# Kernel tuning notes

Measured on AMD Instinct MI355X. Metric: run time of the kernel, lower is better.

The kernel has to match this reference:

```python
import jax, jax.numpy as jnp
import numpy as np

EMBED_DIM = 1024
NUM_HEADS = 16
HEAD_DIM = EMBED_DIM // NUM_HEADS
SCALE = HEAD_DIM ** -0.5


def setup_inputs() -> dict:
    key = jax.random.key(0)
    ks = jax.random.split(key, 11)
    B, T, C = 4, 2048, EMBED_DIM
    s = 1.0 / np.sqrt(C)
    return {
        "query": jax.random.normal(ks[0], (B, T, C), jnp.float32),
        "key": jax.random.normal(ks[1], (B, T, C), jnp.float32),
        "value": jax.random.normal(ks[2], (B, T, C), jnp.float32),
        "Wq": jax.random.normal(ks[3], (C, C), jnp.float32) * s,
        "bq": jnp.zeros((C,), jnp.float32),
        "Wk": jax.random.normal(ks[4], (C, C), jnp.float32) * s,
        "bk": jnp.zeros((C,), jnp.float32),
        "Wv": jax.random.normal(ks[5], (C, C), jnp.float32) * s,
        "bv": jnp.zeros((C,), jnp.float32),
        "Wo": jax.random.normal(ks[6], (C, C), jnp.float32) * s,
        "bo": jnp.zeros((C,), jnp.float32),
    }


def reference(query, key, value, Wq, bq, Wk, bk, Wv, bv, Wo, bo):
    B, Tq, C = query.shape
    Tk = key.shape[1]
    H, D = NUM_HEADS, HEAD_DIM
    # Linear projections (torch Linear: x @ W.T + b), split heads -> (B, H, T, D)
    q = (query @ Wq.T + bq).reshape(B, Tq, H, D).transpose(0, 2, 1, 3)
    k = (key @ Wk.T + bk).reshape(B, Tk, H, D).transpose(0, 2, 1, 3)
    v = (value @ Wv.T + bv).reshape(B, Tk, H, D).transpose(0, 2, 1, 3)
    scores = jnp.einsum("bhqd,bhkd->bhqk", q, k) * SCALE
    attn = jax.nn.softmax(scores, axis=-1)
    out = jnp.einsum("bhqk,bhkd->bhqd", attn, v)
    out = out.transpose(0, 2, 1, 3).reshape(B, Tq, C)
    return out @ Wo.T + bo
```

## Files before the change

kernel.cpp:

```cpp
#include <hip/hip_runtime.h>
#include <stdint.h>
#include <math.h>

#define C_DIM 1024
#define H_NUM 16
#define D_DIM 64
#define B_NUM 4
#define T_SEQ 2048
#define M_ROWS (B_NUM * T_SEQ)

#define SCALE_LOG2E (0.125f * 1.44269504088896340736f)

typedef __attribute__((ext_vector_type(8))) __bf16 bf16x8;
typedef __attribute__((ext_vector_type(2))) __bf16 bf16x2;
typedef __attribute__((ext_vector_type(4))) float f32x4;

__device__ __forceinline__ unsigned short f2bf(float f) {
  union { float f; uint32_t u; } v; v.f = f;
  uint32_t r = v.u + 0x7FFFu + ((v.u >> 16) & 1u);
  return (unsigned short)(r >> 16);
}

__device__ __forceinline__ uint32_t pk2bf(float a, float b) {
#if __has_builtin(__builtin_amdgcn_cvt_pk_bf16_f32)
  union { bf16x2 v; uint32_t u; } u;
  u.v = __builtin_amdgcn_cvt_pk_bf16_f32(a, b);
  return u.u;
#else
  union { float f; uint32_t u; } x, y; x.f = a; y.f = b;
  return __builtin_amdgcn_perm(y.u + 0x8000u, x.u + 0x8000u, 0x07060302u);
#endif
}

__device__ __forceinline__ float frcp(float x) {
#if __has_builtin(__builtin_amdgcn_rcpf)
  return __builtin_amdgcn_rcpf(x);
#else
  return 1.f / x;
#endif
}

__device__ __forceinline__ f32x4 mfma16(bf16x8 a, bf16x8 b, f32x4 c) {
  return __builtin_amdgcn_mfma_f32_16x16x32_bf16(a, b, c, 0, 0, 0);
}

__device__ __forceinline__ void cp16(const void* g, void* l) {
  __builtin_amdgcn_global_load_lds(
      (const __attribute__((address_space(1))) unsigned int*)g,
      (__attribute__((address_space(3))) unsigned int*)l, 16, 0, 0);
}

__global__ __launch_bounds__(256) void cast_all(
    const float* __restrict__ a0, const float* __restrict__ a1,
    const float* __restrict__ a2, const float* __restrict__ w0,
    const float* __restrict__ w1, const float* __restrict__ w2,
    const float* __restrict__ w3, unsigned short* __restrict__ oa0,
    unsigned short* __restrict__ oa1, unsigned short* __restrict__ oa2,
    unsigned short* __restrict__ ow0, unsigned short* __restrict__ ow1,
    unsigned short* __restrict__ ow2, unsigned short* __restrict__ ow3,
    int big4, int small4) {
  int i = blockIdx.x * 256 + threadIdx.x;
  int y = blockIdx.y;
  const float* s;
  unsigned short* d;
  int n4;
  switch (y) {
    case 0: s = a0; d = oa0; n4 = big4; break;
    case 1: s = a1; d = oa1; n4 = big4; break;
    case 2: s = a2; d = oa2; n4 = big4; break;
    case 3: s = w0; d = ow0; n4 = small4; break;
    case 4: s = w1; d = ow1; n4 = small4; break;
    case 5: s = w2; d = ow2; n4 = small4; break;
    default: s = w3; d = ow3; n4 = small4; break;
  }
  if (i >= n4) return;
  float4 v = ((const float4*)s)[i];
  ushort4 o;
  o.x = f2bf(v.x); o.y = f2bf(v.y); o.z = f2bf(v.z); o.w = f2bf(v.w);
  ((ushort4*)d)[i] = o;
}

__device__ __forceinline__ void gemm_tile_128(
    const unsigned short* __restrict__ A, const unsigned short* __restrict__ Bw,
    int row0, int col0, unsigned short* As, unsigned short* Bs, f32x4 acc[4][4]) {
  const int lane = threadIdx.x & 63;
  const int wave = threadIdx.x >> 6;
  const int wm = wave >> 1, wn = wave & 1;
#pragma unroll
  for (int mt = 0; mt < 4; ++mt)
#pragma unroll
    for (int nt = 0; nt < 4; ++nt) acc[mt][nt] = (f32x4){0.f, 0.f, 0.f, 0.f};

  for (int k0 = 0; k0 < C_DIM; k0 += 64) {
    __syncthreads();
#pragma unroll
    for (int rr = 0; rr < 4; ++rr) {
      int c = (rr * 4 + wave) * 64 + lane;
      int row = c >> 3;
      int g = (c & 7) ^ (row & 7);
      cp16(A + (size_t)(row0 + row) * C_DIM + k0 + g * 8, As + (rr * 4 + wave) * 512);
      cp16(Bw + (size_t)(col0 + row) * C_DIM + k0 + g * 8, Bs + (rr * 4 + wave) * 512);
    }
    __syncthreads();
#pragma unroll
    for (int ks = 0; ks < 2; ++ks) {
      bf16x8 af[4], bfr[4];
#pragma unroll
      for (int mt = 0; mt < 4; ++mt) {
        int row = wm * 64 + mt * 16 + (lane & 15);
        int gs = (ks * 4 + (lane >> 4)) ^ (row & 7);
        af[mt] = *(const bf16x8*)(As + row * 64 + gs * 8);
      }
#pragma unroll
      for (int nt = 0; nt < 4; ++nt) {
        int row = wn * 64 + nt * 16 + (lane & 15);
        int gs = (ks * 4 + (lane >> 4)) ^ (row & 7);
        bfr[nt] = *(const bf16x8*)(Bs + row * 64 + gs * 8);
      }
#pragma unroll
      for (int mt = 0; mt < 4; ++mt)
#pragma unroll
        for (int nt = 0; nt < 4; ++nt)
          acc[mt][nt] = mfma16(af[mt], bfr[nt], acc[mt][nt]);
    }
  }
}

__global__ __launch_bounds__(256) void gemm_qkv(
    const unsigned short* __restrict__ qb, const unsigned short* __restrict__ kb,
    const unsigned short* __restrict__ vb, const unsigned short* __restrict__ wq,
    const unsigned short* __restrict__ wk, const unsigned short* __restrict__ wv,
    const float* __restrict__ bq, const float* __restrict__ bk,
    const float* __restrict__ bv, unsigned short* __restrict__ Qp,
    unsigned short* __restrict__ Kp, unsigned short* __restrict__ Vp) {
  __shared__ alignas(16) unsigned short As[128 * 64];
  __shared__ alignas(16) unsigned short Bs[128 * 64];
  const int z = blockIdx.z;
  const unsigned short* A = (z == 0) ? qb : (z == 1) ? kb : vb;
  const unsigned short* W = (z == 0) ? wq : (z == 1) ? wk : wv;
  const float* bias = (z == 0) ? bq : (z == 1) ? bk : bv;
  const int row0 = blockIdx.y * 128, col0 = blockIdx.x * 128;
  f32x4 acc[4][4];
  gemm_tile_128(A, W, row0, col0, As, Bs, acc);

  const int lane = threadIdx.x & 63;
  const int wave = threadIdx.x >> 6;
  const int wm = wave >> 1, wn = wave & 1;
  const int quad = lane >> 4;
#pragma unroll
  for (int mt = 0; mt < 4; ++mt)
#pragma unroll
    for (int nt = 0; nt < 4; ++nt) {
      int n = col0 + wn * 64 + nt * 16 + (lane & 15);
      float bval = bias[n];
      int h = n >> 6, d = n & 63;
      if (z == 2) {
        int m0 = row0 + wm * 64 + mt * 16 + quad * 4;
        int b = m0 >> 11, t0 = m0 & 2047;
        float f0 = acc[mt][nt][0] + bval, f1 = acc[mt][nt][1] + bval;
        float f2 = acc[mt][nt][2] + bval, f3 = acc[mt][nt][3] + bval;
        uint2 pk = {pk2bf(f0, f1), pk2bf(f2, f3)};
        size_t off = (((size_t)(b * H_NUM + h) * (T_SEQ / 8) + (t0 >> 3)) * D_DIM + d) * 8
                     + (t0 & 7);
        *(uint2*)(Vp + off) = pk;
      } else {
#pragma unroll
        for (int r = 0; r < 4; ++r) {
          int m = row0 + wm * 64 + mt * 16 + quad * 4 + r;
          int b = m >> 11, t = m & 2047;
          float f = acc[mt][nt][r] + bval;
          if (z == 0) f *= SCALE_LOG2E;
          unsigned short val = f2bf(f);
          if (z == 0)
            Qp[((size_t)(b * H_NUM + h) * T_SEQ + t) * D_DIM + d] = val;
          else
            Kp[((size_t)(b * H_NUM + h) * T_SEQ + t) * D_DIM + d] = val;
        }
      }
    }
}

__device__ __forceinline__ int fsw(int r) { return (r + ((r >> 3) << 2)) & 7; }

__global__ __launch_bounds__(256, 3) void attn_kernel(
    const unsigned short* __restrict__ Qp, const unsigned short* __restrict__ Kp,
    const unsigned short* __restrict__ Vp, unsigned short* __restrict__ Op) {
  __shared__ alignas(16) unsigned short Ks[2][64 * 64];
  __shared__ alignas(16) unsigned short Vt[2][64 * 64];
  const int bh = blockIdx.x;
  const int q0 = blockIdx.y * 128;
  const int lane = threadIdx.x & 63;
  const int wave = threadIdx.x >> 6;
  const int quad = lane >> 4;
  const int q15 = lane & 15;

  bf16x8 qf[2][2];
#pragma unroll
  for (int g = 0; g < 2; ++g) {
    const unsigned short* qrow =
        Qp + ((size_t)bh * T_SEQ + q0 + wave * 32 + g * 16 + q15) * D_DIM;
    qf[g][0] = *(const bf16x8*)(qrow + quad * 8);
    qf[g][1] = *(const bf16x8*)(qrow + 32 + quad * 8);
  }

  bf16x8 onesf;
#pragma unroll
  for (int i = 0; i < 8; ++i) onesf[i] = (__bf16)1.0f;

  f32x4 oacc[2][4];
  f32x4 lacc[2];
#pragma unroll
  for (int g = 0; g < 2; ++g) {
    lacc[g] = (f32x4){0.f, 0.f, 0.f, 0.f};
#pragma unroll
    for (int dt = 0; dt < 4; ++dt) oacc[g][dt] = (f32x4){0.f, 0.f, 0.f, 0.f};
  }

  const unsigned short* Kbase = Kp + (size_t)bh * T_SEQ * D_DIM;
  const unsigned short* Vbase = Vp + (size_t)bh * T_SEQ * D_DIM;

#define STAGE(kt, buf)                                                        \
  {                                                                           \
    _Pragma("unroll") for (int i = 0; i < 2; ++i) {                           \
      int chunk = wave * 2 + i;                                     \
      int c = chunk * 64 + lane;                                              \
      int row = c >> 3;                                                       \
      int g = (c & 7) ^ fsw(row);                                             \
      cp16(Kbase + ((size_t)((kt) * 64 + row)) * D_DIM + g * 8,               \
           &Ks[buf][chunk * 512]);                                            \
      cp16(Vbase + (size_t)((kt) * 8 + chunk) * 512 + lane * 8,               \
           &Vt[buf][chunk * 512]);                                            \
    }                                                                         \
  }

  STAGE(0, 0);

  for (int kt = 0; kt < T_SEQ / 64; ++kt) {
    const int buf = kt & 1;
    __syncthreads();
    if (kt + 1 < T_SEQ / 64) STAGE(kt + 1, buf ^ 1);

    bf16x8 kfr[4][2];
#pragma unroll
    for (int mt = 0; mt < 4; ++mt) {
      int rowp = 32 * (mt >> 1) + (q15 >> 2) * 8 + (mt & 1) * 4 + (q15 & 3);
#pragma unroll
      for (int ks = 0; ks < 2; ++ks) {
        int gs = (ks * 4 + quad) ^ fsw(rowp);
        kfr[mt][ks] = *(const bf16x8*)(&Ks[buf][rowp * 64 + gs * 8]);
      }
    }
    bf16x8 Pb[2][2];
#pragma unroll
    for (int g = 0; g < 2; ++g) {
      f32x4 s[4];
#pragma unroll
      for (int mt = 0; mt < 4; ++mt) s[mt] = (f32x4){0.f, 0.f, 0.f, 0.f};
#pragma unroll
      for (int ks = 0; ks < 2; ++ks)
#pragma unroll
        for (int mt = 0; mt < 4; ++mt)
          s[mt] = mfma16(kfr[mt][ks], qf[g][ks], s[mt]);
#pragma unroll
      for (int a = 0; a < 2; ++a) {
        float p0 = __builtin_amdgcn_exp2f(s[2 * a][0]);
        float p1 = __builtin_amdgcn_exp2f(s[2 * a][1]);
        float p2 = __builtin_amdgcn_exp2f(s[2 * a][2]);
        float p3 = __builtin_amdgcn_exp2f(s[2 * a][3]);
        float p4 = __builtin_amdgcn_exp2f(s[2 * a + 1][0]);
        float p5 = __builtin_amdgcn_exp2f(s[2 * a + 1][1]);
        float p6 = __builtin_amdgcn_exp2f(s[2 * a + 1][2]);
        float p7 = __builtin_amdgcn_exp2f(s[2 * a + 1][3]);
        union { bf16x8 v; uint32_t u[4]; } pk;
        pk.u[0] = pk2bf(p0, p1);
        pk.u[1] = pk2bf(p2, p3);
        pk.u[2] = pk2bf(p4, p5);
        pk.u[3] = pk2bf(p6, p7);
        Pb[g][a] = pk.v;
      }
    }

#pragma unroll
    for (int a = 0; a < 2; ++a) {
      lacc[0] = mfma16(onesf, Pb[0][a], lacc[0]);
      lacc[1] = mfma16(onesf, Pb[1][a], lacc[1]);
#pragma unroll
      for (int dt = 0; dt < 4; ++dt) {
        bf16x8 vf =
            *(const bf16x8*)(&Vt[buf][((a * 4 + quad) * 64 + dt * 16 + q15) * 8]);
        oacc[0][dt] = mfma16(vf, Pb[0][a], oacc[0][dt]);
        oacc[1][dt] = mfma16(vf, Pb[1][a], oacc[1][dt]);
      }
    }
  }
#undef STAGE

  const int b = bh >> 4, h = bh & 15;
#pragma unroll
  for (int g = 0; g < 2; ++g) {
    float inv = frcp(lacc[g][0]);
    int t = q0 + wave * 32 + g * 16 + q15;
#pragma unroll
    for (int dt = 0; dt < 4; ++dt) {
      uint2 o = {pk2bf(oacc[g][dt][0] * inv, oacc[g][dt][1] * inv),
                 pk2bf(oacc[g][dt][2] * inv, oacc[g][dt][3] * inv)};
      int col = h * D_DIM + dt * 16 + quad * 4;
      *(uint2*)(Op + ((size_t)b * T_SEQ + t) * C_DIM + col) = o;
    }
  }
}

__global__ __launch_bounds__(256) void gemm_out_kernel(
    const unsigned short* __restrict__ Op, const unsigned short* __restrict__ wo,
    const float* __restrict__ bo, float* __restrict__ out) {
  __shared__ alignas(16) unsigned short As[128 * 64];
  __shared__ alignas(16) unsigned short Bs[128 * 64];
  const int row0 = blockIdx.y * 128, col0 = blockIdx.x * 128;
  f32x4 acc[4][4];
  gemm_tile_128(Op, wo, row0, col0, As, Bs, acc);

  const int lane = threadIdx.x & 63;
  const int wave = threadIdx.x >> 6;
  const int wm = wave >> 1, wn = wave & 1;
#pragma unroll
  for (int mt = 0; mt < 4; ++mt)
#pragma unroll
    for (int nt = 0; nt < 4; ++nt) {
      int n = col0 + wn * 64 + nt * 16 + (lane & 15);
      float bval = bo[n];
#pragma unroll
      for (int r = 0; r < 4; ++r) {
        int m = row0 + wm * 64 + mt * 16 + (lane >> 4) * 4 + r;
        out[(size_t)m * C_DIM + n] = acc[mt][nt][r] + bval;
      }
    }
}

extern "C" void kernel_launch(void* const* d_in, const int* in_sizes, int n_in,
                              void* d_out, int out_size, void* d_ws, size_t ws_size,
                              hipStream_t stream) {
  const float* q_in = (const float*)d_in[0];
  const float* k_in = (const float*)d_in[1];
  const float* v_in = (const float*)d_in[2];
  const float* Wq = (const float*)d_in[3];
  const float* bq = (const float*)d_in[4];
  const float* Wk = (const float*)d_in[5];
  const float* bk = (const float*)d_in[6];
  const float* Wv = (const float*)d_in[7];
  const float* bv = (const float*)d_in[8];
  const float* Wo = (const float*)d_in[9];
  const float* bo = (const float*)d_in[10];
  float* out = (float*)d_out;

  const size_t MC = (size_t)M_ROWS * C_DIM;
  const size_t CC = (size_t)C_DIM * C_DIM;
  unsigned short* qb = (unsigned short*)d_ws;
  unsigned short* kb = qb + MC;
  unsigned short* vb = kb + MC;
  unsigned short* wqb = vb + MC;
  unsigned short* wkb = wqb + CC;
  unsigned short* wvb = wkb + CC;
  unsigned short* wob = wvb + CC;
  unsigned short* Qp = wob + CC;
  unsigned short* Kp = Qp + MC;
  unsigned short* Vp = Kp + MC;
  unsigned short* Op = Vp + MC;

  const int big4 = (int)(MC / 4), small4 = (int)(CC / 4);
  cast_all<<<dim3((big4 + 255) / 256, 7), dim3(256), 0, stream>>>(
      q_in, k_in, v_in, Wq, Wk, Wv, Wo, qb, kb, vb, wqb, wkb, wvb, wob,
      big4, small4);

  gemm_qkv<<<dim3(C_DIM / 128, M_ROWS / 128, 3), dim3(256), 0, stream>>>(
      qb, kb, vb, wqb, wkb, wvb, bq, bk, bv, Qp, Kp, Vp);

  attn_kernel<<<dim3(B_NUM * H_NUM, T_SEQ / 128), dim3(256), 0, stream>>>(
      Qp, Kp, Vp, Op);

  gemm_out_kernel<<<dim3(C_DIM / 128, M_ROWS / 128), dim3(256), 0, stream>>>(
      Op, wob, bo, out);
}
```

Before: 334.3 us.

## Double-buffer GEMM LDS tiles, remap block order, transpose Q/K epilogue

The shared GEMM tile loop now uses two LDS buffers, issuing the async copy for the next K-slice before computing on the current one, with a single barrier per iteration so loads overlap MFMA work. Both GEMM kernels remap the linear block index so consecutive blocks share the same weight column tile and spread across row tiles, aiming for better L2 reuse. For Q and K projections the operands are swapped so each lane holds four consecutive head-dim values, allowing packed 8-byte stores and a vectorized bias load instead of scattered 2-byte stores. LDS use doubles to 64KB per block, which may reduce occupancy.

```diff
diff --git a/kernel.cpp b/kernel.cpp
--- a/kernel.cpp
+++ b/kernel.cpp
@@ -91,17 +91,26 @@
 #pragma unroll
     for (int nt = 0; nt < 4; ++nt) acc[mt][nt] = (f32x4){0.f, 0.f, 0.f, 0.f};
 
-  for (int k0 = 0; k0 < C_DIM; k0 += 64) {
+#define GQSTAGE(kk, bb)                                                        \
+  {                                                                            \
+    _Pragma("unroll") for (int rr = 0; rr < 4; ++rr) {                         \
+      int c = (rr * 4 + wave) * 64 + lane;                                     \
+      int row = c >> 3;                                                        \
+      int g = (c & 7) ^ (row & 7);                                             \
+      cp16(A + (size_t)(row0 + row) * C_DIM + (kk) + g * 8,                    \
+           As + (bb) * 8192 + (rr * 4 + wave) * 512);                          \
+      cp16(Bw + (size_t)(col0 + row) * C_DIM + (kk) + g * 8,                   \
+           Bs + (bb) * 8192 + (rr * 4 + wave) * 512);                          \
+    }                                                                          \
+  }
+
+  GQSTAGE(0, 0);
+  for (int it = 0; it < C_DIM / 64; ++it) {
+    const int buf = it & 1;
     __syncthreads();
-#pragma unroll
-    for (int rr = 0; rr < 4; ++rr) {
-      int c = (rr * 4 + wave) * 64 + lane;
-      int row = c >> 3;
-      int g = (c & 7) ^ (row & 7);
-      cp16(A + (size_t)(row0 + row) * C_DIM + k0 + g * 8, As + (rr * 4 + wave) * 512);
-      cp16(Bw + (size_t)(col0 + row) * C_DIM + k0 + g * 8, Bs + (rr * 4 + wave) * 512);
-    }
-    __syncthreads();
+    if (it + 1 < C_DIM / 64) GQSTAGE((it + 1) * 64, buf ^ 1);
+    const unsigned short* Ab = As + buf * 8192;
+    const unsigned short* Bb = Bs + buf * 8192;
 #pragma unroll
     for (int ks = 0; ks < 2; ++ks) {
       bf16x8 af[4], bfr[4];
@@ -109,13 +118,13 @@
       for (int mt = 0; mt < 4; ++mt) {
         int row = wm * 64 + mt * 16 + (lane & 15);
         int gs = (ks * 4 + (lane >> 4)) ^ (row & 7);
-        af[mt] = *(const bf16x8*)(As + row * 64 + gs * 8);
+        af[mt] = *(const bf16x8*)(Ab + row * 64 + gs * 8);
       }
 #pragma unroll
       for (int nt = 0; nt < 4; ++nt) {
         int row = wn * 64 + nt * 16 + (lane & 15);
         int gs = (ks * 4 + (lane >> 4)) ^ (row & 7);
-        bfr[nt] = *(const bf16x8*)(Bs + row * 64 + gs * 8);
+        bfr[nt] = *(const bf16x8*)(Bb + row * 64 + gs * 8);
       }
 #pragma unroll
       for (int mt = 0; mt < 4; ++mt)
@@ -124,6 +133,7 @@
           acc[mt][nt] = mfma16(af[mt], bfr[nt], acc[mt][nt]);
     }
   }
+#undef GQSTAGE
 }
 
 __global__ __launch_bounds__(256) void gemm_qkv(
@@ -133,51 +143,64 @@
     const float* __restrict__ bq, const float* __restrict__ bk,
     const float* __restrict__ bv, unsigned short* __restrict__ Qp,
     unsigned short* __restrict__ Kp, unsigned short* __restrict__ Vp) {
-  __shared__ alignas(16) unsigned short As[128 * 64];
-  __shared__ alignas(16) unsigned short Bs[128 * 64];
-  const int z = blockIdx.z;
+  __shared__ alignas(16) unsigned short As[2][128 * 64];
+  __shared__ alignas(16) unsigned short Bs[2][128 * 64];
+  const int lin = blockIdx.x + 8 * blockIdx.y + 512 * blockIdx.z;
+  const int rowb = ((lin & 7) << 3) | ((lin >> 3) & 7);
+  const int colb = (lin >> 6) & 7;
+  const int z = lin >> 9;
   const unsigned short* A = (z == 0) ? qb : (z == 1) ? kb : vb;
   const unsigned short* W = (z == 0) ? wq : (z == 1) ? wk : wv;
   const float* bias = (z == 0) ? bq : (z == 1) ? bk : bv;
-  const int row0 = blockIdx.y * 128, col0 = blockIdx.x * 128;
-  f32x4 acc[4][4];
-  gemm_tile_128(A, W, row0, col0, As, Bs, acc);
+  const int m0 = rowb * 128, n0 = colb * 128;
 
   const int lane = threadIdx.x & 63;
   const int wave = threadIdx.x >> 6;
   const int wm = wave >> 1, wn = wave & 1;
   const int quad = lane >> 4;
-#pragma unroll
-  for (int mt = 0; mt < 4; ++mt)
-#pragma unroll
-    for (int nt = 0; nt < 4; ++nt) {
-      int n = col0 + wn * 64 + nt * 16 + (lane & 15);
-      float bval = bias[n];
-      int h = n >> 6, d = n & 63;
-      if (z == 2) {
-        int m0 = row0 + wm * 64 + mt * 16 + quad * 4;
-        int b = m0 >> 11, t0 = m0 & 2047;
+  const int q15 = lane & 15;
+  f32x4 acc[4][4];
+
+  if (z == 2) {
+    gemm_tile_128(A, W, m0, n0, &As[0][0], &Bs[0][0], acc);
+#pragma unroll
+    for (int mt = 0; mt < 4; ++mt)
+#pragma unroll
+      for (int nt = 0; nt < 4; ++nt) {
+        int n = n0 + wn * 64 + nt * 16 + q15;
+        float bval = bias[n];
+        int h = n >> 6, d = n & 63;
+        int m0t = m0 + wm * 64 + mt * 16 + quad * 4;
+        int b = m0t >> 11, t0 = m0t & 2047;
         float f0 = acc[mt][nt][0] + bval, f1 = acc[mt][nt][1] + bval;
         float f2 = acc[mt][nt][2] + bval, f3 = acc[mt][nt][3] + bval;
         uint2 pk = {pk2bf(f0, f1), pk2bf(f2, f3)};
         size_t off = (((size_t)(b * H_NUM + h) * (T_SEQ / 8) + (t0 >> 3)) * D_DIM + d) * 8
                      + (t0 & 7);
         *(uint2*)(Vp + off) = pk;
-      } else {
-#pragma unroll
-        for (int r = 0; r < 4; ++r) {
-          int m = row0 + wm * 64 + mt * 16 + quad * 4 + r;
-          int b = m >> 11, t = m & 2047;
-          float f = acc[mt][nt][r] + bval;
-          if (z == 0) f *= SCALE_LOG2E;
-          unsigned short val = f2bf(f);
-          if (z == 0)
-            Qp[((size_t)(b * H_NUM + h) * T_SEQ + t) * D_DIM + d] = val;
-          else
-            Kp[((size_t)(b * H_NUM + h) * T_SEQ + t) * D_DIM + d] = val;
-        }
-      }
-    }
+      }
+  } else {
+    gemm_tile_128(W, A, n0, m0, &As[0][0], &Bs[0][0], acc);
+    unsigned short* dst = (z == 0) ? Qp : Kp;
+    const float sc = (z == 0) ? SCALE_LOG2E : 1.0f;
+#pragma unroll
+    for (int mt = 0; mt < 4; ++mt) {
+      int nb = n0 + wm * 64 + mt * 16 + quad * 4;
+      float4 b4 = *(const float4*)(bias + nb);
+      int h = nb >> 6, d0 = nb & 63;
+#pragma unroll
+      for (int nt = 0; nt < 4; ++nt) {
+        int m = m0 + wn * 64 + nt * 16 + q15;
+        int b = m >> 11, t = m & 2047;
+        float f0 = (acc[mt][nt][0] + b4.x) * sc;
+        float f1 = (acc[mt][nt][1] + b4.y) * sc;
+        float f2 = (acc[mt][nt][2] + b4.z) * sc;
+        float f3 = (acc[mt][nt][3] + b4.w) * sc;
+        uint2 pk = {pk2bf(f0, f1), pk2bf(f2, f3)};
+        *(uint2*)(dst + ((size_t)(b * H_NUM + h) * T_SEQ + t) * D_DIM + d0) = pk;
+      }
+    }
+  }
 }
 
 __device__ __forceinline__ int fsw(int r) { return (r + ((r >> 3) << 2)) & 7; }
@@ -313,11 +336,14 @@
 __global__ __launch_bounds__(256) void gemm_out_kernel(
     const unsigned short* __restrict__ Op, const unsigned short* __restrict__ wo,
     const float* __restrict__ bo, float* __restrict__ out) {
-  __shared__ alignas(16) unsigned short As[128 * 64];
-  __shared__ alignas(16) unsigned short Bs[128 * 64];
-  const int row0 = blockIdx.y * 128, col0 = blockIdx.x * 128;
+  __shared__ alignas(16) unsigned short As[2][128 * 64];
+  __shared__ alignas(16) unsigned short Bs[2][128 * 64];
+  const int lin = blockIdx.x + 8 * blockIdx.y;
+  const int rowb = ((lin & 7) << 3) | ((lin >> 3) & 7);
+  const int colb = (lin >> 6) & 7;
+  const int row0 = rowb * 128, col0 = colb * 128;
   f32x4 acc[4][4];
-  gemm_tile_128(Op, wo, row0, col0, As, Bs, acc);
+  gemm_tile_128(Op, wo, row0, col0, &As[0][0], &Bs[0][0], acc);
 
   const int lane = threadIdx.x & 63;
   const int wave = threadIdx.x >> 6;
```

Result: no change. 328.1 us (-1.9%).
